# Performance work log

Hardware: AMD Instinct MI355X
Metric: run time of the kernel (lower is better)

Reference implementation:

```python
import jax, jax.numpy as jnp
import numpy as np

MASK_VAL = 1e9  # matches torch max_int_value used to force self-pairs to the top
LN_EPS = 1e-5


def setup_inputs() -> dict:
    key = jax.random.key(0)
    kq, kk = jax.random.split(key)
    q = jax.random.normal(kq, (16, 2048, 1024), dtype=jnp.float32)
    k = jax.random.normal(kk, (16, 2048, 1024), dtype=jnp.float32)
    return {"q": q, "k": k, "top_k_instances": 100, "top_k_relationships": 5}


def reference(q, k, top_k_instances, top_k_relationships):
    b, n, d = q.shape
    K, R = top_k_instances, top_k_relationships
    # attention scores [b, n, n]
    scores = jax.nn.softmax(jnp.einsum('bid,bjd->bij', q, k), axis=-1)
    diag = jnp.diagonal(scores, axis1=-2, axis2=-1)            # [b, n]
    _, inst_idx = jax.lax.top_k(diag, K)                        # [b, K]
    inst_idx = jnp.sort(inst_idx, axis=-1)                      # ascending, as torch.sort
    # gather the KxK submatrix of scores restricted to top-K instances
    bidx = jnp.arange(b)[:, None, None]
    rel = scores[bidx, inst_idx[:, :, None], inst_idx[:, None, :]]  # [b, K, K]
    rel = jnp.where(jnp.eye(K, dtype=bool)[None, :, :], MASK_VAL, rel)
    _, rel_idx = jax.lax.top_k(rel, R)                          # [b, K, R]
    # torch.where enumerates the scattered -1s in row-major order with
    # ascending column index per row -> sort topk column indices per row
    cols = jnp.sort(rel_idx, axis=-1).reshape(b, K * R)         # [b, K*R]
    rows = jnp.repeat(jnp.arange(K), R)                         # [K*R], constant
    subj_tok = jnp.take(inst_idx, rows, axis=1)                 # [b, K*R] original token ids
    obj_tok = jnp.take_along_axis(inst_idx, cols, axis=1)       # [b, K*R]
    batch_ids = jnp.broadcast_to(jnp.arange(b)[:, None], (b, K * R))
    subject_object_indices = jnp.stack([batch_ids, subj_tok, obj_tok], axis=-1)  # [b, K*R, 3]
    subject_embeds = jnp.take_along_axis(q, subj_tok[:, :, None], axis=1)  # [b, K*R, d]
    object_embeds = jnp.take_along_axis(q, obj_tok[:, :, None], axis=1)
    x = subject_embeds + object_embeds
    mu = jnp.mean(x, axis=-1, keepdims=True)
    var = jnp.mean((x - mu) ** 2, axis=-1, keepdims=True)
    relationship_embeds = (x - mu) / jnp.sqrt(var + LN_EPS)
    return subject_object_indices, relationship_embeds
```

## Files before the change

kernel.cpp:

```cpp
#include <hip/hip_runtime.h>
#include <math.h>

#define B_ 16
#define N_ 2048
#define D_ 1024
#define KTOP 100
#define RTOP 5
#define JCH 16

typedef __attribute__((ext_vector_type(8))) short short8;
typedef __attribute__((ext_vector_type(4))) float f32x4;

__device__ inline unsigned cvt_pk_bf16(float lo, float hi) {
  unsigned r;
  asm("v_cvt_pk_bf16_f32 %0, %1, %2" : "=v"(r) : "v"(lo), "v"(hi));
  return r;
}
__device__ inline float lo_bf(unsigned p) { return __uint_as_float(p << 16); }
__device__ inline float hi_bf(unsigned p) { return __uint_as_float(p & 0xFFFF0000u); }

__global__ __launch_bounds__(256) void rowstats_mfma(
    const float* __restrict__ q, const float* __restrict__ k,
    float* __restrict__ mpart, float* __restrict__ lpart) {
  __shared__ short Ah[128 * 32], Am[128 * 32];
  __shared__ short Bh[128 * 32], Bm[128 * 32];
  const int tid = threadIdx.x;
  const int wave = tid >> 6, lane = tid & 63;
  const int b = blockIdx.z;
  const int rb = blockIdx.x;
  const int cb = blockIdx.y;
  const float* qb = q + ((size_t)b * N_ + rb * 128) * D_;
  const float* kb = k + ((size_t)b * N_ + cb * 128) * D_;

  const int srow = tid & 127;
  const float* sbase = ((tid < 128) ? qb : kb) + (size_t)srow * D_;
  short* dsth = (tid < 128) ? Ah : Bh;
  short* dstm = (tid < 128) ? Am : Bm;
  const int swz = (srow >> 1) & 3;

  f32x4 acc[2][8];
#pragma unroll
  for (int fr = 0; fr < 2; ++fr)
#pragma unroll
    for (int fc = 0; fc < 8; ++fc)
#pragma unroll
      for (int r = 0; r < 4; ++r) acc[fr][fc][r] = 0.0f;

  const int g = lane >> 4;
  const int rlo = lane & 15;

  for (int kt = 0; kt < D_ / 32; ++kt) {
    __syncthreads();
    {
      const float* src = sbase + kt * 32;
#pragma unroll
      for (int j = 0; j < 4; ++j) {
        float4 ta = ((const float4*)src)[2 * j];
        float4 tb = ((const float4*)src)[2 * j + 1];
        unsigned h0 = cvt_pk_bf16(ta.x, ta.y);
        unsigned h1 = cvt_pk_bf16(ta.z, ta.w);
        unsigned h2 = cvt_pk_bf16(tb.x, tb.y);
        unsigned h3 = cvt_pk_bf16(tb.z, tb.w);
        float r0 = ta.x - lo_bf(h0), r1 = ta.y - hi_bf(h0);
        float r2 = ta.z - lo_bf(h1), r3 = ta.w - hi_bf(h1);
        float r4 = tb.x - lo_bf(h2), r5 = tb.y - hi_bf(h2);
        float r6 = tb.z - lo_bf(h3), r7 = tb.w - hi_bf(h3);
        unsigned m0 = cvt_pk_bf16(r0, r1);
        unsigned m1 = cvt_pk_bf16(r2, r3);
        unsigned m2 = cvt_pk_bf16(r4, r5);
        unsigned m3 = cvt_pk_bf16(r6, r7);
        const int off = srow * 32 + ((j ^ swz) << 3);
        *(int4*)(dsth + off) = make_int4(h0, h1, h2, h3);
        *(int4*)(dstm + off) = make_int4(m0, m1, m2, m3);
      }
    }
    __syncthreads();
    short8 afh[2], afm[2];
#pragma unroll
    for (int fr = 0; fr < 2; ++fr) {
      const int R = (wave << 5) + (fr << 4) + rlo;
      const int off = R * 32 + ((g ^ ((R >> 1) & 3)) << 3);
      afh[fr] = *(const short8*)&Ah[off];
      afm[fr] = *(const short8*)&Am[off];
    }
#pragma unroll
    for (int fc = 0; fc < 8; ++fc) {
      const int Rb = (fc << 4) + rlo;
      const int offb = Rb * 32 + ((g ^ ((Rb >> 1) & 3)) << 3);
      short8 bh = *(const short8*)&Bh[offb];
      short8 bm = *(const short8*)&Bm[offb];
#pragma unroll
      for (int fr = 0; fr < 2; ++fr) {
        acc[fr][fc] = __builtin_amdgcn_mfma_f32_16x16x32_bf16(afh[fr], bh, acc[fr][fc], 0, 0, 0);
        acc[fr][fc] = __builtin_amdgcn_mfma_f32_16x16x32_bf16(afh[fr], bm, acc[fr][fc], 0, 0, 0);
        acc[fr][fc] = __builtin_amdgcn_mfma_f32_16x16x32_bf16(afm[fr], bh, acc[fr][fc], 0, 0, 0);
        acc[fr][fc] = __builtin_amdgcn_mfma_f32_16x16x32_bf16(afm[fr], bm, acc[fr][fc], 0, 0, 0);
      }
    }
  }

#pragma unroll
  for (int fr = 0; fr < 2; ++fr) {
#pragma unroll
    for (int r = 0; r < 4; ++r) {
      float vmax = acc[fr][0][r];
#pragma unroll
      for (int fc = 1; fc < 8; ++fc) vmax = fmaxf(vmax, acc[fr][fc][r]);
#pragma unroll
      for (int m = 1; m < 16; m <<= 1) vmax = fmaxf(vmax, __shfl_xor(vmax, m));
      float s = 0.0f;
#pragma unroll
      for (int fc = 0; fc < 8; ++fc) s += __expf(acc[fr][fc][r] - vmax);
#pragma unroll
      for (int m = 1; m < 16; m <<= 1) s += __shfl_xor(s, m);
      if ((lane & 15) == 0) {
        const int row = (wave << 5) + (fr << 4) + ((lane >> 4) << 2) + r;
        size_t o = ((size_t)b * JCH + cb) * N_ + rb * 128 + row;
        mpart[o] = vmax;
        lpart[o] = s;
      }
    }
  }
}

__global__ __launch_bounds__(256) void combine_kernel(
    const float* __restrict__ mpart, const float* __restrict__ lpart,
    float* __restrict__ mfin, float* __restrict__ lfin) {
  int r = blockIdx.x * 256 + threadIdx.x;
  int b = r >> 11;
  int i = r & (N_ - 1);
  float m = -INFINITY, l = 0.0f;
  for (int jc = 0; jc < JCH; ++jc) {
    size_t o = ((size_t)b * JCH + jc) * N_ + i;
    float mp = mpart[o], lp = lpart[o];
    float mn = fmaxf(m, mp);
    l = l * __expf(m - mn) + lp * __expf(mp - mn);
    m = mn;
  }
  mfin[r] = m;
  lfin[r] = l;
}

__global__ __launch_bounds__(256) void diag_kernel(
    const float* __restrict__ q, const float* __restrict__ k,
    const float* __restrict__ mfin, const float* __restrict__ lfin,
    float* __restrict__ diag) {
  int wave = threadIdx.x >> 6, lane = threadIdx.x & 63;
  int row = blockIdx.x * 4 + wave;
  int b = row >> 11, i = row & (N_ - 1);
  const float* qr = q + ((size_t)b * N_ + i) * D_;
  const float* kr = k + ((size_t)b * N_ + i) * D_;
  float s = 0.0f;
  for (int t = 0; t < D_ / 64; ++t) s = fmaf(qr[lane + (t << 6)], kr[lane + (t << 6)], s);
  for (int m = 1; m < 64; m <<= 1) s += __shfl_xor(s, m);
  if (lane == 0) diag[row] = __expf(s - mfin[row]) / lfin[row];
}

__global__ __launch_bounds__(256) void top100_kernel(
    const float* __restrict__ diag, int* __restrict__ inst_idx) {
  __shared__ float sval[N_];
  __shared__ int sidx[N_];
  __shared__ int top[128];
  int b = blockIdx.x, tid = threadIdx.x;
  for (int i = tid; i < N_; i += 256) { sval[i] = diag[(size_t)b * N_ + i]; sidx[i] = i; }
  __syncthreads();
  for (int ksz = 2; ksz <= N_; ksz <<= 1) {
    for (int j = ksz >> 1; j > 0; j >>= 1) {
      for (int t = tid; t < N_; t += 256) {
        int x = t ^ j;
        if (x > t) {
          float va = sval[t], vb = sval[x];
          int ia = sidx[t], ib = sidx[x];
          bool agtb = (va > vb) || (va == vb && ia < ib);
          bool up = ((t & ksz) == 0);
          if (up != agtb) { sval[t] = vb; sval[x] = va; sidx[t] = ib; sidx[x] = ia; }
        }
      }
      __syncthreads();
    }
  }
  if (tid < 128) top[tid] = (tid < KTOP) ? sidx[tid] : 0x7FFFFFFF;
  __syncthreads();
  for (int ksz = 2; ksz <= 128; ksz <<= 1) {
    for (int j = ksz >> 1; j > 0; j >>= 1) {
      if (tid < 128) {
        int t = tid, x = t ^ j;
        if (x > t) {
          int ia = top[t], ib = top[x];
          bool up = ((t & ksz) == 0);
          bool altb = ia < ib;
          if (up != altb) { top[t] = ib; top[x] = ia; }
        }
      }
      __syncthreads();
    }
  }
  if (tid < KTOP) inst_idx[b * KTOP + tid] = top[tid];
}

__global__ __launch_bounds__(256) void reltop_kernel(
    const float* __restrict__ q, const float* __restrict__ k,
    const float* __restrict__ mfin, const float* __restrict__ lfin,
    const int* __restrict__ inst_idx, float* __restrict__ out0,
    int* __restrict__ pairs) {
  __shared__ int inst[KTOP];
  __shared__ float qv[D_];
  __shared__ float sv[KTOP];
  int a = blockIdx.x, b = blockIdx.y, tid = threadIdx.x;
  if (tid < KTOP) inst[tid] = inst_idx[b * KTOP + tid];
  __syncthreads();
  int ia = inst[a];
  const float* qrow = q + ((size_t)b * N_ + ia) * D_;
  for (int t = tid; t < D_; t += 256) qv[t] = qrow[t];
  __syncthreads();
  int wave = tid >> 6, lane = tid & 63;
  for (int c0 = 0; c0 < KTOP; c0 += 4) {
    int c = c0 + wave;
    const float* krow = k + ((size_t)b * N_ + inst[c]) * D_;
    float s = 0.0f;
    for (int t = 0; t < D_ / 64; ++t) s = fmaf(qv[lane + (t << 6)], krow[lane + (t << 6)], s);
    for (int m = 1; m < 64; m <<= 1) s += __shfl_xor(s, m);
    if (lane == 0) sv[c] = s;
  }
  __syncthreads();
  if (tid < 64) {
    float mi = mfin[(size_t)b * N_ + ia];
    float li = lfin[(size_t)b * N_ + ia];
    float c0v = (tid == a) ? 1e9f : __expf(sv[tid] - mi) / li;
    int c0i = tid;
    float c1v = -1.0f;
    int c1i = 1 << 20;
    if (tid + 64 < KTOP) {
      c1v = (tid + 64 == a) ? 1e9f : __expf(sv[tid + 64] - mi) / li;
      c1i = tid + 64;
    }
    int sel[RTOP];
    for (int rr = 0; rr < RTOP; ++rr) {
      float v;
      int idx;
      if (c1v > c0v || (c1v == c0v && c1i < c0i)) { v = c1v; idx = c1i; }
      else { v = c0v; idx = c0i; }
      for (int m = 1; m < 64; m <<= 1) {
        float ov = __shfl_xor(v, m);
        int oi = __shfl_xor(idx, m);
        if (ov > v || (ov == v && oi < idx)) { v = ov; idx = oi; }
      }
      sel[rr] = idx;
      if (idx == c0i) c0v = -2.0f;
      if (idx == c1i) c1v = -2.0f;
    }
    if (lane == 0) {
      for (int i2 = 0; i2 < RTOP; ++i2)
        for (int j2 = 0; j2 < RTOP - 1 - i2; ++j2)
          if (sel[j2] > sel[j2 + 1]) { int tswap = sel[j2]; sel[j2] = sel[j2 + 1]; sel[j2 + 1] = tswap; }
      for (int rr = 0; rr < RTOP; ++rr) {
        size_t ri = (size_t)b * KTOP * RTOP + (size_t)a * RTOP + rr;
        out0[ri * 3 + 0] = (float)b;
        out0[ri * 3 + 1] = (float)ia;
        out0[ri * 3 + 2] = (float)inst[sel[rr]];
        pairs[ri * 2 + 0] = ia;
        pairs[ri * 2 + 1] = inst[sel[rr]];
      }
    }
  }
}

__global__ __launch_bounds__(256) void embed_kernel(
    const float* __restrict__ q, const int* __restrict__ pairs,
    float* __restrict__ out1) {
  __shared__ float red[8];
  int r = blockIdx.x, b = blockIdx.y, tid = threadIdx.x;
  size_t ri = (size_t)b * KTOP * RTOP + r;
  int subj = pairs[ri * 2 + 0], obj = pairs[ri * 2 + 1];
  const float* qs = q + ((size_t)b * N_ + subj) * D_;
  const float* qo = q + ((size_t)b * N_ + obj) * D_;
  float4 v1 = *(const float4*)(qs + tid * 4);
  float4 v2 = *(const float4*)(qo + tid * 4);
  float x0 = v1.x + v2.x, x1 = v1.y + v2.y, x2 = v1.z + v2.z, x3 = v1.w + v2.w;
  float s = x0 + x1 + x2 + x3;
  float qq = x0 * x0 + x1 * x1 + x2 * x2 + x3 * x3;
  int lane = tid & 63, wave = tid >> 6;
  for (int m = 1; m < 64; m <<= 1) { s += __shfl_xor(s, m); qq += __shfl_xor(qq, m); }
  if (lane == 0) { red[wave] = s; red[4 + wave] = qq; }
  __syncthreads();
  float S = red[0] + red[1] + red[2] + red[3];
  float Q = red[4] + red[5] + red[6] + red[7];
  float mu = S * (1.0f / D_);
  float var = Q * (1.0f / D_) - mu * mu;
  float rstd = 1.0f / sqrtf(var + 1e-5f);
  float4 o;
  o.x = (x0 - mu) * rstd;
  o.y = (x1 - mu) * rstd;
  o.z = (x2 - mu) * rstd;
  o.w = (x3 - mu) * rstd;
  *(float4*)(out1 + ri * D_ + tid * 4) = o;
}

extern "C" void kernel_launch(void* const* d_in, const int* in_sizes, int n_in,
                              void* d_out, int out_size, void* d_ws, size_t ws_size,
                              hipStream_t stream) {
  (void)in_sizes; (void)n_in; (void)out_size; (void)ws_size;
  const float* q = (const float*)d_in[0];
  const float* k = (const float*)d_in[1];
  float* out = (float*)d_out;

  char* ws = (char*)d_ws;
  float* mpart = (float*)ws; ws += (size_t)B_ * JCH * N_ * 4;
  float* lpart = (float*)ws; ws += (size_t)B_ * JCH * N_ * 4;
  float* mfin = (float*)ws;  ws += (size_t)B_ * N_ * 4;
  float* lfin = (float*)ws;  ws += (size_t)B_ * N_ * 4;
  float* diag = (float*)ws;  ws += (size_t)B_ * N_ * 4;
  int* inst = (int*)ws;      ws += (size_t)B_ * KTOP * 4;
  int* pairs = (int*)ws;

  hipLaunchKernelGGL(rowstats_mfma, dim3(N_ / 128, N_ / 128, B_), dim3(256), 0, stream,
                     q, k, mpart, lpart);
  hipLaunchKernelGGL(combine_kernel, dim3(B_ * N_ / 256), dim3(256), 0, stream,
                     mpart, lpart, mfin, lfin);
  hipLaunchKernelGGL(diag_kernel, dim3(B_ * N_ / 4), dim3(256), 0, stream,
                     q, k, mfin, lfin, diag);
  hipLaunchKernelGGL(top100_kernel, dim3(B_), dim3(256), 0, stream, diag, inst);
  hipLaunchKernelGGL(reltop_kernel, dim3(KTOP, B_), dim3(256), 0, stream,
                     q, k, mfin, lfin, inst, out, pairs);
  hipLaunchKernelGGL(embed_kernel, dim3(KTOP * RTOP, B_), dim3(256), 0, stream,
                     q, pairs, out + (size_t)B_ * KTOP * RTOP * 3);
}
```

Measured before the change: 995.0 us.

## Double-buffer LDS tiles and prefetch next K-slice during MFMA in rowstats

Doubles the shared-memory tiles for the hi/lo bf16 split of q and k, and issues global loads for the next 32-wide K slice before the MFMA loop on the current slice. The split and LDS write for the next slice happen after the MFMAs, which removes one barrier per iteration. The aim is to hide global-load latency behind tensor-core work. In exchange it doubles LDS use (64KB per block), which may reduce occupancy, and adds 32 live registers for the prefetched data.

```diff
diff --git a/kernel.cpp b/kernel.cpp
--- a/kernel.cpp
+++ b/kernel.cpp
@@ -19,11 +19,35 @@
 __device__ inline float lo_bf(unsigned p) { return __uint_as_float(p << 16); }
 __device__ inline float hi_bf(unsigned p) { return __uint_as_float(p & 0xFFFF0000u); }
 
+__device__ inline void split_write(const float4* t8, short* dsth, short* dstm,
+                                   int srow, int swz) {
+#pragma unroll
+  for (int j = 0; j < 4; ++j) {
+    float4 ta = t8[2 * j];
+    float4 tb = t8[2 * j + 1];
+    unsigned h0 = cvt_pk_bf16(ta.x, ta.y);
+    unsigned h1 = cvt_pk_bf16(ta.z, ta.w);
+    unsigned h2 = cvt_pk_bf16(tb.x, tb.y);
+    unsigned h3 = cvt_pk_bf16(tb.z, tb.w);
+    float r0 = ta.x - lo_bf(h0), r1 = ta.y - hi_bf(h0);
+    float r2 = ta.z - lo_bf(h1), r3 = ta.w - hi_bf(h1);
+    float r4 = tb.x - lo_bf(h2), r5 = tb.y - hi_bf(h2);
+    float r6 = tb.z - lo_bf(h3), r7 = tb.w - hi_bf(h3);
+    unsigned m0 = cvt_pk_bf16(r0, r1);
+    unsigned m1 = cvt_pk_bf16(r2, r3);
+    unsigned m2 = cvt_pk_bf16(r4, r5);
+    unsigned m3 = cvt_pk_bf16(r6, r7);
+    const int off = srow * 32 + ((j ^ swz) << 3);
+    *(int4*)(dsth + off) = make_int4(h0, h1, h2, h3);
+    *(int4*)(dstm + off) = make_int4(m0, m1, m2, m3);
+  }
+}
+
 __global__ __launch_bounds__(256) void rowstats_mfma(
     const float* __restrict__ q, const float* __restrict__ k,
     float* __restrict__ mpart, float* __restrict__ lpart) {
-  __shared__ short Ah[128 * 32], Am[128 * 32];
-  __shared__ short Bh[128 * 32], Bm[128 * 32];
+  __shared__ short Ah[2][128 * 32], Am[2][128 * 32];
+  __shared__ short Bh[2][128 * 32], Bm[2][128 * 32];
   const int tid = threadIdx.x;
   const int wave = tid >> 6, lane = tid & 63;
   const int b = blockIdx.z;
@@ -34,8 +58,7 @@
 
   const int srow = tid & 127;
   const float* sbase = ((tid < 128) ? qb : kb) + (size_t)srow * D_;
-  short* dsth = (tid < 128) ? Ah : Bh;
-  short* dstm = (tid < 128) ? Am : Bm;
+  const int isB = (tid >> 7);
   const int swz = (srow >> 1) & 3;
 
   f32x4 acc[2][8];
@@ -49,46 +72,40 @@
   const int g = lane >> 4;
   const int rlo = lane & 15;
 
+  {
+    float4 pre[8];
+#pragma unroll
+    for (int i = 0; i < 8; ++i) pre[i] = ((const float4*)sbase)[i];
+    split_write(pre, isB ? Bh[0] : Ah[0], isB ? Bm[0] : Am[0], srow, swz);
+  }
+
   for (int kt = 0; kt < D_ / 32; ++kt) {
     __syncthreads();
-    {
-      const float* src = sbase + kt * 32;
-#pragma unroll
-      for (int j = 0; j < 4; ++j) {
-        float4 ta = ((const float4*)src)[2 * j];
-        float4 tb = ((const float4*)src)[2 * j + 1];
-        unsigned h0 = cvt_pk_bf16(ta.x, ta.y);
-        unsigned h1 = cvt_pk_bf16(ta.z, ta.w);
-        unsigned h2 = cvt_pk_bf16(tb.x, tb.y);
-        unsigned h3 = cvt_pk_bf16(tb.z, tb.w);
-        float r0 = ta.x - lo_bf(h0), r1 = ta.y - hi_bf(h0);
-        float r2 = ta.z - lo_bf(h1), r3 = ta.w - hi_bf(h1);
-        float r4 = tb.x - lo_bf(h2), r5 = tb.y - hi_bf(h2);
-        float r6 = tb.z - lo_bf(h3), r7 = tb.w - hi_bf(h3);
-        unsigned m0 = cvt_pk_bf16(r0, r1);
-        unsigned m1 = cvt_pk_bf16(r2, r3);
-        unsigned m2 = cvt_pk_bf16(r4, r5);
-        unsigned m3 = cvt_pk_bf16(r6, r7);
-        const int off = srow * 32 + ((j ^ swz) << 3);
-        *(int4*)(dsth + off) = make_int4(h0, h1, h2, h3);
-        *(int4*)(dstm + off) = make_int4(m0, m1, m2, m3);
-      }
-    }
-    __syncthreads();
+    const int cur = kt & 1, nxt = cur ^ 1;
+    float4 pre[8];
+    if (kt < D_ / 32 - 1) {
+      const float* src = sbase + (kt + 1) * 32;
+#pragma unroll
+      for (int i = 0; i < 8; ++i) pre[i] = ((const float4*)src)[i];
+    }
+    const short* ahb = Ah[cur];
+    const short* amb = Am[cur];
+    const short* bhb = Bh[cur];
+    const short* bmb = Bm[cur];
     short8 afh[2], afm[2];
 #pragma unroll
     for (int fr = 0; fr < 2; ++fr) {
       const int R = (wave << 5) + (fr << 4) + rlo;
       const int off = R * 32 + ((g ^ ((R >> 1) & 3)) << 3);
-      afh[fr] = *(const short8*)&Ah[off];
-      afm[fr] = *(const short8*)&Am[off];
+      afh[fr] = *(const short8*)&ahb[off];
+      afm[fr] = *(const short8*)&amb[off];
     }
 #pragma unroll
     for (int fc = 0; fc < 8; ++fc) {
       const int Rb = (fc << 4) + rlo;
       const int offb = Rb * 32 + ((g ^ ((Rb >> 1) & 3)) << 3);
-      short8 bh = *(const short8*)&Bh[offb];
-      short8 bm = *(const short8*)&Bm[offb];
+      short8 bh = *(const short8*)&bhb[offb];
+      short8 bm = *(const short8*)&bmb[offb];
 #pragma unroll
       for (int fr = 0; fr < 2; ++fr) {
         acc[fr][fc] = __builtin_amdgcn_mfma_f32_16x16x32_bf16(afh[fr], bh, acc[fr][fc], 0, 0, 0);
@@ -96,6 +113,9 @@
         acc[fr][fc] = __builtin_amdgcn_mfma_f32_16x16x32_bf16(afm[fr], bh, acc[fr][fc], 0, 0, 0);
         acc[fr][fc] = __builtin_amdgcn_mfma_f32_16x16x32_bf16(afm[fr], bm, acc[fr][fc], 0, 0, 0);
       }
+    }
+    if (kt < D_ / 32 - 1) {
+      split_write(pre, isB ? Bh[nxt] : Ah[nxt], isB ? Bm[nxt] : Am[nxt], srow, swz);
     }
   }
 
```

Result: slower. 1.056 ms (+6.2%).
